# Optimization experiments

Measured on AMD Instinct MI355X. Metric: run time of the kernel, lower is better.

Reference implementation:

```python
import jax, jax.numpy as jnp
import numpy as np

SIGMA = 1.0
DELTA = 1.0
TOPK = 10
TOPK_HALF = int(np.around(TOPK / 2))  # 5
EPS = 1e-12


def _cdist(a, b):
    # Euclidean distance matrix, grad-safe sqrt at zero (matches torch.cdist values).
    d2 = (jnp.sum(a * a, axis=1)[:, None]
          + jnp.sum(b * b, axis=1)[None, :]
          - 2.0 * (a @ b.T))
    d2 = jnp.maximum(d2, 0.0)
    pos = d2 > 0.0
    return jnp.where(pos, jnp.sqrt(jnp.where(pos, d2, 1.0)), 0.0)


def _consistency_weights(t_emb):
    # Everything here is under torch.no_grad() in the original.
    N = t_emb.shape[0]
    T_dist = _cdist(t_emb, t_emb)
    W_P = jnp.exp(-(T_dist ** 2) / SIGMA)
    _, idx = jax.lax.top_k(W_P, TOPK)                      # [N, TOPK]
    rows = jnp.arange(N)[:, None]
    W_NN = jnp.zeros_like(W_P).at[rows, idx].set(1.0)      # scatter_ ones
    V = (((W_NN + W_NN.T) / 2) == 1.0).astype(W_P.dtype)   # mutual kNN (symmetric)
    # Vectorized form of the per-row python loop:
    #   W_C_tilda[i, j] = V[i, j] * (sum_k V[i, k] * V[j, k]) / sum_k V[i, k]
    deg = jnp.sum(V, axis=1)                               # >= 1 (self is always a NN)
    overlap = V @ V.T                                      # [N, N] neighbor overlap
    W_C_tilda = V * overlap / deg[:, None]
    topk_half_index = idx[:, :TOPK_HALF]                   # [N, TOPK_HALF]
    W_C_hat = jnp.mean(W_C_tilda[topk_half_index], axis=1) # gather rows, mean -> [N, N]
    W_C = (W_C_hat + W_C_hat.T) / 2
    return (W_P + W_C) / 2


def reference(s_emb, t_emb):
    # disable_mu = 0 -> s_emb NOT normalized; t_emb always normalized.
    t_norm = t_emb / jnp.maximum(
        jnp.linalg.norm(t_emb, axis=1, keepdims=True), EPS)
    N = s_emb.shape[0]
    S_dist = _cdist(s_emb, s_emb)
    S_dist = S_dist / jnp.mean(S_dist, axis=1, keepdims=True)
    W = jax.lax.stop_gradient(_consistency_weights(t_norm))
    off_diag = 1.0 - jnp.eye(N, dtype=W.dtype)
    pos_weight = W * off_diag
    neg_weight = (1.0 - W) * off_diag
    pull = jnp.maximum(S_dist, 0.0) ** 2 * pos_weight
    push = jnp.maximum(DELTA - S_dist, 0.0) ** 2 * neg_weight
    return (jnp.sum(pull) + jnp.sum(push)) / (N * (N - 1))


def setup_inputs() -> dict:
    key = jax.random.key(0)
    k1, k2 = jax.random.split(key)
    N, D = 2048, 1024
    return {
        "s_emb": jax.random.normal(k1, (N, D), dtype=jnp.float32),
        "t_emb": jax.random.normal(k2, (N, D), dtype=jnp.float32),
    }
```

## Files before the change

kernel.cpp:

```cpp
#include <hip/hip_runtime.h>
#include <math.h>

#define N_ 2048
#define D_ 1024
#define TOPK 10
#define TOPK_HALF 5

typedef __attribute__((ext_vector_type(8))) short short8;
typedef __attribute__((ext_vector_type(4))) float floatx4;

__device__ __forceinline__ short f2bf(float f) {
  unsigned u = __float_as_uint(f);
  unsigned r = (u + 0x7fffu + ((u >> 16) & 1u)) >> 16;
  return (short)r;
}

__device__ __forceinline__ void gld_lds16(const short* g, short* l) {
  __builtin_amdgcn_global_load_lds(
      (const __attribute__((address_space(1))) unsigned int*)(g),
      (__attribute__((address_space(3))) unsigned int*)(l), 16, 0, 0);
}

__global__ __launch_bounds__(256) void tnorm_kernel(const float* __restrict__ t,
                                                    short* __restrict__ tb,
                                                    float* __restrict__ tt) {
  int row = blockIdx.x;
  const float* rp = t + (size_t)row * D_;
  short* op = tb + (size_t)row * D_;
  __shared__ float red[256];
  int tid = threadIdx.x;
  float s = 0.f;
  for (int k = tid; k < D_; k += 256) { float v = rp[k]; s += v * v; }
  red[tid] = s; __syncthreads();
  for (int st = 128; st > 0; st >>= 1) { if (tid < st) red[tid] += red[tid + st]; __syncthreads(); }
  float denom = fmaxf(sqrtf(red[0]), 1e-12f);
  __syncthreads();
  float s2 = 0.f;
  for (int k = tid; k < D_; k += 256) { float v = rp[k] / denom; op[k] = f2bf(v); s2 += v * v; }
  red[tid] = s2; __syncthreads();
  for (int st = 128; st > 0; st >>= 1) { if (tid < st) red[tid] += red[tid + st]; __syncthreads(); }
  if (tid == 0) tt[row] = red[0];
}

__global__ __launch_bounds__(256) void sconv_kernel(const float* __restrict__ a,
                                                    short* __restrict__ ab,
                                                    float* __restrict__ out) {
  int row = blockIdx.x;
  const float* rp = a + (size_t)row * D_;
  short* op = ab + (size_t)row * D_;
  __shared__ float red[256];
  int tid = threadIdx.x;
  float s = 0.f;
  for (int k = tid; k < D_; k += 256) { float v = rp[k]; op[k] = f2bf(v); s += v * v; }
  red[tid] = s; __syncthreads();
  for (int st = 128; st > 0; st >>= 1) { if (tid < st) red[tid] += red[tid + st]; __syncthreads(); }
  if (tid == 0) out[row] = red[0];
}

__global__ __launch_bounds__(256) void gram_mfma_kernel(
    const short* __restrict__ Tb, const short* __restrict__ Sb,
    const float* __restrict__ tt, const float* __restrict__ ss,
    float* __restrict__ WP, float* __restrict__ Sout) {
  const int mode = blockIdx.z;
  const short* A = mode ? Sb : Tb;
  const float* rn = mode ? ss : tt;
  float* out = mode ? Sout : WP;

  __shared__ __align__(16) short As[128 * 64];
  __shared__ __align__(16) short Bs[128 * 64];

  int tid = threadIdx.x;
  int w = tid >> 6, lane = tid & 63;
  int i0 = blockIdx.y * 128, j0 = blockIdx.x * 128;
  int wr = w >> 1, wc = w & 1;
  int quad = lane >> 4, l16 = lane & 15;

  floatx4 acc[4][4] = {};

  int srow = w * 32 + (lane >> 3);
  int scol = (lane & 7) * 8;
  const short* Ag = A + (size_t)(i0 + srow) * D_ + scol;
  const short* Bg = A + (size_t)(j0 + srow) * D_ + scol;
  short* Al = As + srow * 64 + scol;
  short* Bl = Bs + srow * 64 + scol;

  for (int k0 = 0; k0 < D_; k0 += 64) {
    __syncthreads();
#pragma unroll
    for (int q = 0; q < 4; q++) {
      gld_lds16(Ag + k0 + (size_t)q * 8 * D_, Al + q * 8 * 64);
      gld_lds16(Bg + k0 + (size_t)q * 8 * D_, Bl + q * 8 * 64);
    }
    __syncthreads();
#pragma unroll
    for (int ks = 0; ks < 64; ks += 32) {
      short8 af[4], bfr[4];
#pragma unroll
      for (int mt = 0; mt < 4; mt++)
        af[mt] = *(const short8*)&As[(wr * 64 + mt * 16 + l16) * 64 + ks + quad * 8];
#pragma unroll
      for (int nt = 0; nt < 4; nt++)
        bfr[nt] = *(const short8*)&Bs[(wc * 64 + nt * 16 + l16) * 64 + ks + quad * 8];
#pragma unroll
      for (int mt = 0; mt < 4; mt++)
#pragma unroll
        for (int nt = 0; nt < 4; nt++)
          acc[mt][nt] = __builtin_amdgcn_mfma_f32_16x16x32_bf16(af[mt], bfr[nt], acc[mt][nt], 0, 0, 0);
    }
  }

#pragma unroll
  for (int mt = 0; mt < 4; mt++) {
    int ib = i0 + wr * 64 + mt * 16 + quad * 4;
#pragma unroll
    for (int r = 0; r < 4; r++) {
      int i = ib + r;
      float ri = rn[i];
#pragma unroll
      for (int nt = 0; nt < 4; nt++) {
        int j = j0 + wc * 64 + nt * 16 + l16;
        float d2 = fmaxf(ri + rn[j] - 2.f * acc[mt][nt][r], 0.f);
        float o = (mode == 0) ? expf(-d2) : sqrtf(d2);
        if (i == j) o = (mode == 0) ? 1.f : 0.f;
        out[(size_t)i * N_ + j] = o;
      }
    }
  }
}

__global__ __launch_bounds__(256) void topk_kernel(const float* __restrict__ W_P,
                                                   int* __restrict__ idx) {
  int row = blockIdx.x;
  __shared__ float vals[N_];
  __shared__ float wv[4];
  __shared__ int wi[4];
  int tid = threadIdx.x;
  const float* rp = W_P + (size_t)row * N_;
  for (int j = tid; j < N_; j += 256) vals[j] = rp[j];
  __syncthreads();
  for (int t = 0; t < TOPK; t++) {
    float bv = -2.f; int bi = N_;
    for (int j = tid; j < N_; j += 256) {
      float v = vals[j];
      if (v > bv) { bv = v; bi = j; }
    }
#pragma unroll
    for (int off = 32; off > 0; off >>= 1) {
      float ov = __shfl_down(bv, off);
      int oi = __shfl_down(bi, off);
      if (ov > bv || (ov == bv && oi < bi)) { bv = ov; bi = oi; }
    }
    int w = tid >> 6;
    if ((tid & 63) == 0) { wv[w] = bv; wi[w] = bi; }
    __syncthreads();
    if (tid == 0) {
      float b0 = wv[0]; int i0 = wi[0];
#pragma unroll
      for (int u = 1; u < 4; u++)
        if (wv[u] > b0 || (wv[u] == b0 && wi[u] < i0)) { b0 = wv[u]; i0 = wi[u]; }
      idx[row * TOPK + t] = i0;
      vals[i0] = -1.f;
    }
    __syncthreads();
  }
}

__global__ void mutual_kernel(const int* __restrict__ idx, int* __restrict__ nbr,
                              int* __restrict__ deg) {
  int i = blockIdx.x * blockDim.x + threadIdx.x;
  if (i >= N_) return;
  int cnt = 0;
  for (int k = 0; k < TOPK; k++) {
    int j = idx[i * TOPK + k];
    bool mut = false;
    for (int l = 0; l < TOPK; l++)
      if (idx[j * TOPK + l] == i) mut = true;
    if (mut) nbr[i * TOPK + cnt++] = j;
  }
  deg[i] = cnt;
}

__global__ void overlap_kernel(const int* __restrict__ nbr, const int* __restrict__ deg,
                               float* __restrict__ ovl) {
  int t = blockIdx.x * blockDim.x + threadIdx.x;
  int i = t / TOPK, k = t % TOPK;
  if (i >= N_) return;
  int di = deg[i];
  if (k >= di) return;
  int j = nbr[i * TOPK + k];
  int dj = deg[j];
  int c = 0;
  for (int a = 0; a < di; a++) {
    int na = nbr[i * TOPK + a];
    for (int b = 0; b < dj; b++) c += (nbr[j * TOPK + b] == na);
  }
  ovl[i * TOPK + k] = (float)c;
}

__global__ __launch_bounds__(256) void rowmean_kernel(const float* __restrict__ S,
                                                      float* __restrict__ rowmean) {
  int row = blockIdx.x;
  const float4* rp = (const float4*)(S + (size_t)row * N_);
  __shared__ float red[256];
  int tid = threadIdx.x;
  float s = 0.f;
  for (int j = tid; j < N_ / 4; j += 256) { float4 v = rp[j]; s += v.x + v.y + v.z + v.w; }
  red[tid] = s; __syncthreads();
  for (int st = 128; st > 0; st >>= 1) { if (tid < st) red[tid] += red[tid + st]; __syncthreads(); }
  if (tid == 0) rowmean[row] = red[0] / (float)N_;
}

__global__ __launch_bounds__(256) void loss_kernel(const float* __restrict__ W_P,
                                                   const float* __restrict__ S,
                                                   const float* __restrict__ rowmean,
                                                   float* __restrict__ partials) {
  int i = blockIdx.x;
  int tid = threadIdx.x;
  float rminv = 1.f / rowmean[i];
  const float4* wpr = (const float4*)(W_P + (size_t)i * N_);
  const float4* sr = (const float4*)(S + (size_t)i * N_);
  float local = 0.f;
  for (int j4 = tid; j4 < N_ / 4; j4 += 256) {
    float4 wp = wpr[j4], sv = sr[j4];
#pragma unroll
    for (int c = 0; c < 4; c++) {
      float s = ((const float*)&sv)[c] * rminv;
      float d = fmaxf(1.0f - s, 0.f);
      local += d * d + 0.5f * ((const float*)&wp)[c] * (s * s - d * d);
    }
  }
  __shared__ float red[256];
  red[tid] = local; __syncthreads();
  for (int st = 128; st > 0; st >>= 1) { if (tid < st) red[tid] += red[tid + st]; __syncthreads(); }
  if (tid == 0) partials[i] = red[0] - 0.5f;
}

__global__ __launch_bounds__(256) void sparse_wc_kernel(
    const int* __restrict__ idx, const int* __restrict__ nbr,
    const int* __restrict__ deg, const float* __restrict__ ovl,
    const float* __restrict__ S, const float* __restrict__ rowmean,
    float* __restrict__ sparse_partials) {
  int t = blockIdx.x * 256 + threadIdx.x;
  int i = t / (TOPK_HALF * TOPK);
  int r = t % (TOPK_HALF * TOPK);
  int mi = r / TOPK, k = r % TOPK;
  float contrib = 0.f;
  if (i < N_) {
    int m = idx[i * TOPK + mi];
    int dm = deg[m];
    if (k < dm) {
      int col = nbr[m * TOPK + k];
      if (col != i) {
        float v = ovl[m * TOPK + k] / (float)dm * 0.1f;
        float s1 = S[(size_t)i * N_ + col] / rowmean[i];
        float d1 = fmaxf(1.f - s1, 0.f);
        float s2 = S[(size_t)col * N_ + i] / rowmean[col];
        float d2 = fmaxf(1.f - s2, 0.f);
        contrib = 0.5f * v * ((s1 * s1 - d1 * d1) + (s2 * s2 - d2 * d2));
      }
    }
  }
  __shared__ float red[256];
  red[threadIdx.x] = contrib; __syncthreads();
  for (int st = 128; st > 0; st >>= 1) {
    if (threadIdx.x < st) red[threadIdx.x] += red[threadIdx.x + st];
    __syncthreads();
  }
  if (threadIdx.x == 0) sparse_partials[blockIdx.x] = red[0];
}

#define SPARSE_BLOCKS ((N_ * TOPK_HALF * TOPK) / 256)

__global__ __launch_bounds__(256) void finalize_kernel(const float* __restrict__ partials,
                                                       const float* __restrict__ sparse_partials,
                                                       float* __restrict__ out) {
  __shared__ float red[256];
  int tid = threadIdx.x;
  float s = 0.f;
  for (int i = tid; i < N_; i += 256) s += partials[i];
  for (int i = tid; i < SPARSE_BLOCKS; i += 256) s += sparse_partials[i];
  red[tid] = s; __syncthreads();
  for (int st = 128; st > 0; st >>= 1) { if (tid < st) red[tid] += red[tid + st]; __syncthreads(); }
  if (tid == 0) out[0] = red[0] / ((float)N_ * (float)(N_ - 1));
}

extern "C" void kernel_launch(void* const* d_in, const int* in_sizes, int n_in,
                              void* d_out, int out_size, void* d_ws, size_t ws_size,
                              hipStream_t stream) {
  const float* s_emb = (const float*)d_in[0];
  const float* t_emb = (const float*)d_in[1];
  float* out = (float*)d_out;

  const size_t NN = (size_t)N_ * N_;
  const size_t ND = (size_t)N_ * D_;
  short* t_bf = (short*)d_ws;
  short* s_bf = t_bf + ND;
  float* W_P = (float*)(s_bf + ND);
  float* S_raw = W_P + NN;
  float* tt = S_raw + NN;
  float* ss = tt + N_;
  float* rowmean = ss + N_;
  float* partials = rowmean + N_;
  float* sparse_partials = partials + N_;
  float* ovl = sparse_partials + SPARSE_BLOCKS;
  int* idx = (int*)(ovl + (size_t)N_ * TOPK);
  int* nbr = idx + (size_t)N_ * TOPK;
  int* deg = nbr + (size_t)N_ * TOPK;

  tnorm_kernel<<<N_, 256, 0, stream>>>(t_emb, t_bf, tt);
  sconv_kernel<<<N_, 256, 0, stream>>>(s_emb, s_bf, ss);

  dim3 g(N_ / 128, N_ / 128, 2);
  gram_mfma_kernel<<<g, 256, 0, stream>>>(t_bf, s_bf, tt, ss, W_P, S_raw);

  topk_kernel<<<N_, 256, 0, stream>>>(W_P, idx);
  mutual_kernel<<<N_ / 256, 256, 0, stream>>>(idx, nbr, deg);
  overlap_kernel<<<(N_ * TOPK + 255) / 256, 256, 0, stream>>>(nbr, deg, ovl);

  rowmean_kernel<<<N_, 256, 0, stream>>>(S_raw, rowmean);
  loss_kernel<<<N_, 256, 0, stream>>>(W_P, S_raw, rowmean, partials);
  sparse_wc_kernel<<<SPARSE_BLOCKS, 256, 0, stream>>>(idx, nbr, deg, ovl, S_raw, rowmean,
                                                      sparse_partials);
  finalize_kernel<<<1, 256, 0, stream>>>(partials, sparse_partials, out);
}
```

Before: 162.5 us.

## Fuse pipeline stages, store distance matrices in bf16, accumulate loss atomically

Merges the two input-prep kernels into one launch. The row means of S are now computed in the gram epilogue using wave shuffles and atomics. Top-k is fused with the dense loss, which reads each row once from registers. The overlap computation moves into the sparse kernel, and the finalize pass is replaced by atomic accumulation into the output. The two N×N matrices are stored as bf16 instead of fp32, halving their write and read traffic. In exchange, top-k now selects on bf16-rounded weights, so neighbor choice can change under near-ties, and the float atomics make the summation order nondeterministic.

```diff
diff --git a/kernel.cpp b/kernel.cpp
--- a/kernel.cpp
+++ b/kernel.cpp
@@ -5,6 +5,7 @@
 #define D_ 1024
 #define TOPK 10
 #define TOPK_HALF 5
+#define INV_NORM (1.0f / ((float)N_ * (float)(N_ - 1)))
 
 typedef __attribute__((ext_vector_type(8))) short short8;
 typedef __attribute__((ext_vector_type(4))) float floatx4;
@@ -14,6 +15,9 @@
   unsigned r = (u + 0x7fffu + ((u >> 16) & 1u)) >> 16;
   return (short)r;
 }
+__device__ __forceinline__ float bf2f(short b) {
+  return __uint_as_float(((unsigned)(unsigned short)b) << 16);
+}
 
 __device__ __forceinline__ void gld_lds16(const short* g, short* l) {
   __builtin_amdgcn_global_load_lds(
@@ -21,50 +25,55 @@
       (__attribute__((address_space(3))) unsigned int*)(l), 16, 0, 0);
 }
 
-__global__ __launch_bounds__(256) void tnorm_kernel(const float* __restrict__ t,
-                                                    short* __restrict__ tb,
-                                                    float* __restrict__ tt) {
-  int row = blockIdx.x;
-  const float* rp = t + (size_t)row * D_;
-  short* op = tb + (size_t)row * D_;
+__global__ __launch_bounds__(256) void prep_kernel(const float* __restrict__ t,
+                                                   const float* __restrict__ s,
+                                                   short* __restrict__ tb,
+                                                   short* __restrict__ sb,
+                                                   float* __restrict__ tt,
+                                                   float* __restrict__ ss,
+                                                   float* __restrict__ rowsum,
+                                                   float* __restrict__ out) {
+  int b = blockIdx.x, tid = threadIdx.x;
   __shared__ float red[256];
-  int tid = threadIdx.x;
-  float s = 0.f;
-  for (int k = tid; k < D_; k += 256) { float v = rp[k]; s += v * v; }
-  red[tid] = s; __syncthreads();
-  for (int st = 128; st > 0; st >>= 1) { if (tid < st) red[tid] += red[tid + st]; __syncthreads(); }
-  float denom = fmaxf(sqrtf(red[0]), 1e-12f);
-  __syncthreads();
-  float s2 = 0.f;
-  for (int k = tid; k < D_; k += 256) { float v = rp[k] / denom; op[k] = f2bf(v); s2 += v * v; }
-  red[tid] = s2; __syncthreads();
-  for (int st = 128; st > 0; st >>= 1) { if (tid < st) red[tid] += red[tid + st]; __syncthreads(); }
-  if (tid == 0) tt[row] = red[0];
-}
-
-__global__ __launch_bounds__(256) void sconv_kernel(const float* __restrict__ a,
-                                                    short* __restrict__ ab,
-                                                    float* __restrict__ out) {
-  int row = blockIdx.x;
-  const float* rp = a + (size_t)row * D_;
-  short* op = ab + (size_t)row * D_;
-  __shared__ float red[256];
-  int tid = threadIdx.x;
-  float s = 0.f;
-  for (int k = tid; k < D_; k += 256) { float v = rp[k]; op[k] = f2bf(v); s += v * v; }
-  red[tid] = s; __syncthreads();
-  for (int st = 128; st > 0; st >>= 1) { if (tid < st) red[tid] += red[tid + st]; __syncthreads(); }
-  if (tid == 0) out[row] = red[0];
+  if (b == 0) {
+    for (int j = tid; j < N_; j += 256) rowsum[j] = 0.f;
+    if (tid == 0) out[0] = 0.f;
+  }
+  if (b < N_) {
+    const float* rp = t + (size_t)b * D_;
+    short* op = tb + (size_t)b * D_;
+    float acc = 0.f;
+    for (int k = tid; k < D_; k += 256) { float v = rp[k]; acc += v * v; }
+    red[tid] = acc; __syncthreads();
+    for (int st = 128; st > 0; st >>= 1) { if (tid < st) red[tid] += red[tid + st]; __syncthreads(); }
+    float denom = fmaxf(sqrtf(red[0]), 1e-12f);
+    __syncthreads();
+    float s2 = 0.f;
+    for (int k = tid; k < D_; k += 256) { float v = rp[k] / denom; op[k] = f2bf(v); s2 += v * v; }
+    red[tid] = s2; __syncthreads();
+    for (int st = 128; st > 0; st >>= 1) { if (tid < st) red[tid] += red[tid + st]; __syncthreads(); }
+    if (tid == 0) tt[b] = red[0];
+  } else {
+    int row = b - N_;
+    const float* rp = s + (size_t)row * D_;
+    short* op = sb + (size_t)row * D_;
+    float acc = 0.f;
+    for (int k = tid; k < D_; k += 256) { float v = rp[k]; op[k] = f2bf(v); acc += v * v; }
+    red[tid] = acc; __syncthreads();
+    for (int st = 128; st > 0; st >>= 1) { if (tid < st) red[tid] += red[tid + st]; __syncthreads(); }
+    if (tid == 0) ss[row] = red[0];
+  }
 }
 
 __global__ __launch_bounds__(256) void gram_mfma_kernel(
     const short* __restrict__ Tb, const short* __restrict__ Sb,
     const float* __restrict__ tt, const float* __restrict__ ss,
-    float* __restrict__ WP, float* __restrict__ Sout) {
+    short* __restrict__ WPb, short* __restrict__ Sob,
+    float* __restrict__ rowsum) {
   const int mode = blockIdx.z;
   const short* A = mode ? Sb : Tb;
   const float* rn = mode ? ss : tt;
-  float* out = mode ? Sout : WP;
+  short* outb = mode ? Sob : WPb;
 
   __shared__ __align__(16) short As[128 * 64];
   __shared__ __align__(16) short Bs[128 * 64];
@@ -111,57 +120,74 @@
 
 #pragma unroll
   for (int mt = 0; mt < 4; mt++) {
-    int ib = i0 + wr * 64 + mt * 16 + quad * 4;
 #pragma unroll
     for (int r = 0; r < 4; r++) {
-      int i = ib + r;
+      int i = i0 + wr * 64 + mt * 16 + quad * 4 + r;
       float ri = rn[i];
+      float rs = 0.f;
 #pragma unroll
       for (int nt = 0; nt < 4; nt++) {
         int j = j0 + wc * 64 + nt * 16 + l16;
         float d2 = fmaxf(ri + rn[j] - 2.f * acc[mt][nt][r], 0.f);
-        float o = (mode == 0) ? expf(-d2) : sqrtf(d2);
-        if (i == j) o = (mode == 0) ? 1.f : 0.f;
-        out[(size_t)i * N_ + j] = o;
+        float o = mode ? sqrtf(d2) : expf(-d2);
+        if (i == j) o = mode ? 0.f : 1.f;
+        outb[(size_t)i * N_ + j] = f2bf(o);
+        rs += o;
       }
-    }
-  }
-}
-
-__global__ __launch_bounds__(256) void topk_kernel(const float* __restrict__ W_P,
-                                                   int* __restrict__ idx) {
-  int row = blockIdx.x;
-  __shared__ float vals[N_];
+      if (mode) {
+        rs += __shfl_xor(rs, 1); rs += __shfl_xor(rs, 2);
+        rs += __shfl_xor(rs, 4); rs += __shfl_xor(rs, 8);
+        if (l16 == 0) atomicAdd(&rowsum[i], rs);
+      }
+    }
+  }
+}
+
+__global__ __launch_bounds__(256) void topk_loss_kernel(const short* __restrict__ WPb,
+                                                        const short* __restrict__ Sb,
+                                                        const float* __restrict__ rowsum,
+                                                        int* __restrict__ idx,
+                                                        float* __restrict__ out) {
+  int row = blockIdx.x, tid = threadIdx.x;
+  short8 wp8 = ((const short8*)(WPb + (size_t)row * N_))[tid];
+  short8 s8 = ((const short8*)(Sb + (size_t)row * N_))[tid];
+  float w[8];
+  float rminv = (float)N_ / rowsum[row];
+  float local = 0.f;
+#pragma unroll
+  for (int c = 0; c < 8; c++) {
+    w[c] = bf2f(wp8[c]);
+    float sv = bf2f(s8[c]) * rminv;
+    float d = fmaxf(1.0f - sv, 0.f);
+    local += d * d + 0.5f * w[c] * (sv * sv - d * d);
+  }
+  __shared__ float red[256];
   __shared__ float wv[4];
   __shared__ int wi[4];
-  int tid = threadIdx.x;
-  const float* rp = W_P + (size_t)row * N_;
-  for (int j = tid; j < N_; j += 256) vals[j] = rp[j];
-  __syncthreads();
+  red[tid] = local; __syncthreads();
+  for (int st = 128; st > 0; st >>= 1) { if (tid < st) red[tid] += red[tid + st]; __syncthreads(); }
+  if (tid == 0) atomicAdd(out, (red[0] - 0.5f) * INV_NORM);
+
   for (int t = 0; t < TOPK; t++) {
-    float bv = -2.f; int bi = N_;
-    for (int j = tid; j < N_; j += 256) {
-      float v = vals[j];
-      if (v > bv) { bv = v; bi = j; }
-    }
+    float bv = -2.f; int bi = 0;
+#pragma unroll
+    for (int c = 0; c < 8; c++)
+      if (w[c] > bv) { bv = w[c]; bi = tid * 8 + c; }
 #pragma unroll
     for (int off = 32; off > 0; off >>= 1) {
       float ov = __shfl_down(bv, off);
       int oi = __shfl_down(bi, off);
       if (ov > bv || (ov == bv && oi < bi)) { bv = ov; bi = oi; }
     }
-    int w = tid >> 6;
-    if ((tid & 63) == 0) { wv[w] = bv; wi[w] = bi; }
-    __syncthreads();
-    if (tid == 0) {
-      float b0 = wv[0]; int i0 = wi[0];
-#pragma unroll
-      for (int u = 1; u < 4; u++)
-        if (wv[u] > b0 || (wv[u] == b0 && wi[u] < i0)) { b0 = wv[u]; i0 = wi[u]; }
-      idx[row * TOPK + t] = i0;
-      vals[i0] = -1.f;
-    }
-    __syncthreads();
+    __syncthreads();
+    if ((tid & 63) == 0) { wv[tid >> 6] = bv; wi[tid >> 6] = bi; }
+    __syncthreads();
+    float b0 = wv[0]; int j0w = wi[0];
+#pragma unroll
+    for (int u = 1; u < 4; u++)
+      if (wv[u] > b0 || (wv[u] == b0 && wi[u] < j0w)) { b0 = wv[u]; j0w = wi[u]; }
+    if (tid == 0) idx[row * TOPK + t] = j0w;
+    if ((j0w >> 3) == tid) w[j0w & 7] = -1.f;
   }
 }
 
@@ -180,66 +206,10 @@
   deg[i] = cnt;
 }
 
-__global__ void overlap_kernel(const int* __restrict__ nbr, const int* __restrict__ deg,
-                               float* __restrict__ ovl) {
-  int t = blockIdx.x * blockDim.x + threadIdx.x;
-  int i = t / TOPK, k = t % TOPK;
-  if (i >= N_) return;
-  int di = deg[i];
-  if (k >= di) return;
-  int j = nbr[i * TOPK + k];
-  int dj = deg[j];
-  int c = 0;
-  for (int a = 0; a < di; a++) {
-    int na = nbr[i * TOPK + a];
-    for (int b = 0; b < dj; b++) c += (nbr[j * TOPK + b] == na);
-  }
-  ovl[i * TOPK + k] = (float)c;
-}
-
-__global__ __launch_bounds__(256) void rowmean_kernel(const float* __restrict__ S,
-                                                      float* __restrict__ rowmean) {
-  int row = blockIdx.x;
-  const float4* rp = (const float4*)(S + (size_t)row * N_);
-  __shared__ float red[256];
-  int tid = threadIdx.x;
-  float s = 0.f;
-  for (int j = tid; j < N_ / 4; j += 256) { float4 v = rp[j]; s += v.x + v.y + v.z + v.w; }
-  red[tid] = s; __syncthreads();
-  for (int st = 128; st > 0; st >>= 1) { if (tid < st) red[tid] += red[tid + st]; __syncthreads(); }
-  if (tid == 0) rowmean[row] = red[0] / (float)N_;
-}
-
-__global__ __launch_bounds__(256) void loss_kernel(const float* __restrict__ W_P,
-                                                   const float* __restrict__ S,
-                                                   const float* __restrict__ rowmean,
-                                                   float* __restrict__ partials) {
-  int i = blockIdx.x;
-  int tid = threadIdx.x;
-  float rminv = 1.f / rowmean[i];
-  const float4* wpr = (const float4*)(W_P + (size_t)i * N_);
-  const float4* sr = (const float4*)(S + (size_t)i * N_);
-  float local = 0.f;
-  for (int j4 = tid; j4 < N_ / 4; j4 += 256) {
-    float4 wp = wpr[j4], sv = sr[j4];
-#pragma unroll
-    for (int c = 0; c < 4; c++) {
-      float s = ((const float*)&sv)[c] * rminv;
-      float d = fmaxf(1.0f - s, 0.f);
-      local += d * d + 0.5f * ((const float*)&wp)[c] * (s * s - d * d);
-    }
-  }
-  __shared__ float red[256];
-  red[tid] = local; __syncthreads();
-  for (int st = 128; st > 0; st >>= 1) { if (tid < st) red[tid] += red[tid + st]; __syncthreads(); }
-  if (tid == 0) partials[i] = red[0] - 0.5f;
-}
-
 __global__ __launch_bounds__(256) void sparse_wc_kernel(
     const int* __restrict__ idx, const int* __restrict__ nbr,
-    const int* __restrict__ deg, const float* __restrict__ ovl,
-    const float* __restrict__ S, const float* __restrict__ rowmean,
-    float* __restrict__ sparse_partials) {
+    const int* __restrict__ deg, const short* __restrict__ Sb,
+    const float* __restrict__ rowsum, float* __restrict__ out) {
   int t = blockIdx.x * 256 + threadIdx.x;
   int i = t / (TOPK_HALF * TOPK);
   int r = t % (TOPK_HALF * TOPK);
@@ -251,10 +221,16 @@
     if (k < dm) {
       int col = nbr[m * TOPK + k];
       if (col != i) {
-        float v = ovl[m * TOPK + k] / (float)dm * 0.1f;
-        float s1 = S[(size_t)i * N_ + col] / rowmean[i];
+        int dj = deg[col];
+        int c = 0;
+        for (int a = 0; a < dm; a++) {
+          int na = nbr[m * TOPK + a];
+          for (int b = 0; b < dj; b++) c += (nbr[col * TOPK + b] == na);
+        }
+        float v = (float)c / (float)dm * 0.1f;
+        float s1 = bf2f(Sb[(size_t)i * N_ + col]) * ((float)N_ / rowsum[i]);
         float d1 = fmaxf(1.f - s1, 0.f);
-        float s2 = S[(size_t)col * N_ + i] / rowmean[col];
+        float s2 = bf2f(Sb[(size_t)col * N_ + i]) * ((float)N_ / rowsum[col]);
         float d2 = fmaxf(1.f - s2, 0.f);
         contrib = 0.5f * v * ((s1 * s1 - d1 * d1) + (s2 * s2 - d2 * d2));
       }
@@ -266,23 +242,10 @@
     if (threadIdx.x < st) red[threadIdx.x] += red[threadIdx.x + st];
     __syncthreads();
   }
-  if (threadIdx.x == 0) sparse_partials[blockIdx.x] = red[0];
+  if (threadIdx.x == 0) atomicAdd(out, red[0] * INV_NORM);
 }
 
 #define SPARSE_BLOCKS ((N_ * TOPK_HALF * TOPK) / 256)
-
-__global__ __launch_bounds__(256) void finalize_kernel(const float* __restrict__ partials,
-                                                       const float* __restrict__ sparse_partials,
-                                                       float* __restrict__ out) {
-  __shared__ float red[256];
-  int tid = threadIdx.x;
-  float s = 0.f;
-  for (int i = tid; i < N_; i += 256) s += partials[i];
-  for (int i = tid; i < SPARSE_BLOCKS; i += 256) s += sparse_partials[i];
-  red[tid] = s; __syncthreads();
-  for (int st = 128; st > 0; st >>= 1) { if (tid < st) red[tid] += red[tid + st]; __syncthreads(); }
-  if (tid == 0) out[0] = red[0] / ((float)N_ * (float)(N_ - 1));
-}
 
 extern "C" void kernel_launch(void* const* d_in, const int* in_sizes, int n_in,
                               void* d_out, int out_size, void* d_ws, size_t ws_size,
@@ -295,31 +258,21 @@
   const size_t ND = (size_t)N_ * D_;
   short* t_bf = (short*)d_ws;
   short* s_bf = t_bf + ND;
-  float* W_P = (float*)(s_bf + ND);
-  float* S_raw = W_P + NN;
-  float* tt = S_raw + NN;
+  short* WPb = s_bf + ND;
+  short* Sb = WPb + NN;
+  float* tt = (float*)(Sb + NN);
   float* ss = tt + N_;
-  float* rowmean = ss + N_;
-  float* partials = rowmean + N_;
-  float* sparse_partials = partials + N_;
-  float* ovl = sparse_partials + SPARSE_BLOCKS;
-  int* idx = (int*)(ovl + (size_t)N_ * TOPK);
+  float* rowsum = ss + N_;
+  int* idx = (int*)(rowsum + N_);
   int* nbr = idx + (size_t)N_ * TOPK;
   int* deg = nbr + (size_t)N_ * TOPK;
 
-  tnorm_kernel<<<N_, 256, 0, stream>>>(t_emb, t_bf, tt);
-  sconv_kernel<<<N_, 256, 0, stream>>>(s_emb, s_bf, ss);
+  prep_kernel<<<2 * N_, 256, 0, stream>>>(t_emb, s_emb, t_bf, s_bf, tt, ss, rowsum, out);
 
   dim3 g(N_ / 128, N_ / 128, 2);
-  gram_mfma_kernel<<<g, 256, 0, stream>>>(t_bf, s_bf, tt, ss, W_P, S_raw);
-
-  topk_kernel<<<N_, 256, 0, stream>>>(W_P, idx);
+  gram_mfma_kernel<<<g, 256, 0, stream>>>(t_bf, s_bf, tt, ss, WPb, Sb, rowsum);
+
+  topk_loss_kernel<<<N_, 256, 0, stream>>>(WPb, Sb, rowsum, idx, out);
   mutual_kernel<<<N_ / 256, 256, 0, stream>>>(idx, nbr, deg);
-  overlap_kernel<<<(N_ * TOPK + 255) / 256, 256, 0, stream>>>(nbr, deg, ovl);
-
-  rowmean_kernel<<<N_, 256, 0, stream>>>(S_raw, rowmean);
-  loss_kernel<<<N_, 256, 0, stream>>>(W_P, S_raw, rowmean, partials);
-  sparse_wc_kernel<<<SPARSE_BLOCKS, 256, 0, stream>>>(idx, nbr, deg, ovl, S_raw, rowmean,
-                                                      sparse_partials);
-  finalize_kernel<<<1, 256, 0, stream>>>(partials, sparse_partials, out);
-}
+  sparse_wc_kernel<<<SPARSE_BLOCKS, 256, 0, stream>>>(idx, nbr, deg, Sb, rowsum, out);
+}
```

Result: slower. 172.0 us (+5.8%).
